# Optimization experiments

Measured on AMD Instinct MI355X. Metric: run time of the kernel, lower is better.

The kernel has to match this reference:

```python
import jax, jax.numpy as jnp
import numpy as np

B, L, D = 8, 4096, 256
G, K = 64, 8          # n_groups, group_size
N = G * K             # 512 slots
H = 8                 # attention heads
EPS = 1e-5

def _ln(x, g, b):
    m = jnp.mean(x, axis=-1, keepdims=True)
    v = jnp.var(x, axis=-1, keepdims=True)
    return (x - m) * jax.lax.rsqrt(v + EPS) * g + b

def _gelu(x):
    return jax.nn.gelu(x, approximate=False)  # torch nn.GELU default = exact erf

def setup_inputs() -> dict:
    key = jax.random.key(0)
    ks = jax.random.split(key, 24)
    s = 0.02
    d = {
        'X': jax.random.normal(ks[0], (B, L, D), jnp.float32),
        'S': jax.random.normal(ks[1], (B, N, D), jnp.float32),
        'Wg':  jax.random.normal(ks[2], (D, G)) * s,
        'Wk':  jax.random.normal(ks[3], (D, K)) * s,
        'Wm1': jax.random.normal(ks[4], (D, 2*D)) * s, 'bm1': jnp.zeros((2*D,)),
        'Wm2': jax.random.normal(ks[5], (2*D, D)) * s, 'bm2': jnp.zeros((D,)),
        'Wgt1': jax.random.normal(ks[6], (D, D)) * s, 'bgt1': jnp.zeros((D,)),
        'Wgt2': jax.random.normal(ks[7], (D, 1)) * s, 'bgt2': jnp.zeros((1,)),
        'Wqkv': jax.random.normal(ks[8], (D, 3*D)) * s, 'bqkv': jnp.zeros((3*D,)),
        'Wo':  jax.random.normal(ks[9], (D, D)) * s, 'bo': jnp.zeros((D,)),
        'aln_g': jnp.ones((D,)), 'aln_b': jnp.zeros((D,)),
        'Wu1': jax.random.normal(ks[10], (2*D, 2*D)) * s, 'bu1': jnp.zeros((2*D,)),
        'Wu2': jax.random.normal(ks[11], (2*D, D)) * s, 'bu2': jnp.zeros((D,)),
        'ln_g': jnp.ones((D,)), 'ln_b': jnp.zeros((D,)),
    }
    return d

def reference(X, S, Wg, Wk, Wm1, bm1, Wm2, bm2, Wgt1, bgt1, Wgt2, bgt2,
              Wqkv, bqkv, Wo, bo, aln_g, aln_b, Wu1, bu1, Wu2, bu2, ln_g, ln_b):
    # --- hierarchical routing (eval path: argmax one-hot) ---
    msg = _gelu(X @ Wm1 + bm1) @ Wm2 + bm2                 # (B,L,D)
    gate = jax.nn.sigmoid(_gelu(X @ Wgt1 + bgt1) @ Wgt2 + bgt2)  # (B,L,1)
    gm = msg * gate
    gidx = jnp.argmax(X @ Wg, axis=-1)                     # (B,L)
    kidx = jnp.argmax(X @ Wk, axis=-1)                     # (B,L)
    idx = gidx * K + kidx                                  # flat slot id in [0,N)
    full = jax.nn.one_hot(idx, N, dtype=X.dtype)           # (B,L,N)
    incoming = jnp.einsum('bln,bld->bnd', full, gm)        # (B,N,D)
    # --- slot self-attention ---
    qkv = S @ Wqkv + bqkv
    q, k, v = jnp.split(qkv, 3, axis=-1)
    dh = D // H
    q = q.reshape(B, N, H, dh); k = k.reshape(B, N, H, dh); v = v.reshape(B, N, H, dh)
    scores = jnp.einsum('bqhd,bkhd->bhqk', q, k) / jnp.sqrt(jnp.asarray(dh, X.dtype))
    attn = jax.nn.softmax(scores, axis=-1)
    o = jnp.einsum('bhqk,bkhd->bqhd', attn, v).reshape(B, N, D) @ Wo + bo
    S1 = _ln(S + o, aln_g, aln_b)
    # --- update ---
    cat = jnp.concatenate([S1, incoming], axis=-1)         # (B,N,2D)
    S2 = S1 + _gelu(cat @ Wu1 + bu1) @ Wu2 + bu2
    return _ln(S2, ln_g, ln_b)
```

## Files before the change

kernel.cpp:

```cpp
#include <hip/hip_runtime.h>

typedef __bf16 bf16_t;
typedef __bf16 bf16x8 __attribute__((ext_vector_type(8)));
typedef __bf16 bf16x4v __attribute__((ext_vector_type(4)));
typedef __bf16 bf16x2v __attribute__((ext_vector_type(2)));
typedef float f32x4 __attribute__((ext_vector_type(4)));
typedef unsigned long long u64;

#define LN_EPS 1e-5f

__device__ __forceinline__ float erf_fast(float a) {
  const float t = fabsf(a);
  const float s = a * a;
  float r;
  if (t > 0.921875f) {
    float u;
    r = fmaf(-1.72853470e-5f, t, 3.83197126e-4f);
    u = fmaf(-3.88396438e-3f, t, 2.42546219e-2f);
    r = fmaf(r, s, u);
    r = fmaf(r, t, 1.06777877e-1f);
    r = fmaf(r, t, -6.37245935e-1f);
    r = fmaf(r, t, -1.28717512e-1f);
    r = fmaf(r, t, t);
    r = 1.0f - __expf(-r);
    r = copysignf(r, a);
  } else {
    r = -5.96761703e-4f;
    r = fmaf(r, s, 4.99119423e-3f);
    r = fmaf(r, s, -2.67681349e-2f);
    r = fmaf(r, s, 1.12819925e-1f);
    r = fmaf(r, s, -3.76125336e-1f);
    r = fmaf(r, s, 1.28379166e-1f);
    r = fmaf(r, a, a);
  }
  return r;
}

__device__ __forceinline__ float gelu_f(float x) {
  const float h = 0.5f * x;
  return fmaf(h, erf_fast(x * 0.70710678118654752f), h);
}

__device__ __forceinline__ void async16(const bf16_t* g, bf16_t* l) {
  __builtin_amdgcn_global_load_lds(
      (const __attribute__((address_space(1))) void*)g,
      (__attribute__((address_space(3))) void*)l, 16, 0, 0);
}

__device__ __forceinline__ int swz(int row, int p) { return p ^ ((row >> 1) & 3); }

__global__ __launch_bounds__(256)
void prep_kernel(const float* __restrict__ X, const float* __restrict__ S,
                 const float* __restrict__ Wg, const float* __restrict__ Wk,
                 const float* __restrict__ Wm1, const float* __restrict__ Wgt1,
                 const float* __restrict__ Wm2, const float* __restrict__ Wqkv,
                 const float* __restrict__ Wo, const float* __restrict__ Wu1,
                 const float* __restrict__ Wu2,
                 bf16_t* __restrict__ Xb, bf16_t* __restrict__ Sb,
                 bf16_t* __restrict__ W1t, bf16_t* __restrict__ W2t,
                 bf16_t* __restrict__ Wqkvt, bf16_t* __restrict__ Wot,
                 bf16_t* __restrict__ Wu1t, bf16_t* __restrict__ Wu2t,
                 float4* __restrict__ zbase)
{
  const int bid = blockIdx.x;
  const int t = threadIdx.x;
  if (bid < 8192) {
    const int i = bid * 256 + t;
    const float4 v = ((const float4*)X)[i];
    bf16x4v o; o[0]=(bf16_t)v.x; o[1]=(bf16_t)v.y; o[2]=(bf16_t)v.z; o[3]=(bf16_t)v.w;
    ((bf16x4v*)Xb)[i] = o;
  } else if (bid < 9216) {
    const int i = (bid - 8192) * 256 + t;
    const float4 v = ((const float4*)S)[i];
    bf16x4v o; o[0]=(bf16_t)v.x; o[1]=(bf16_t)v.y; o[2]=(bf16_t)v.z; o[3]=(bf16_t)v.w;
    ((bf16x4v*)Sb)[i] = o;
  } else if (bid < 10112) {
    const int n = bid - 9216;
    const int k = t;
    float v;
    if (n < 512)      v = Wm1[k * 512 + n];
    else if (n < 768) v = Wgt1[k * 256 + (n - 512)];
    else if (n < 832) v = Wg[k * 64 + (n - 768)];
    else if (n < 840) v = Wk[k * 8 + (n - 832)];
    else              v = 0.f;
    W1t[n * 256 + k] = (bf16_t)v;
  } else if (bid < 10368) {
    const int n = bid - 10112;
    for (int k = t; k < 512; k += 256) W2t[n * 512 + k] = (bf16_t)Wm2[k * 256 + n];
  } else if (bid < 11136) {
    const int n = bid - 10368;
    Wqkvt[n * 256 + t] = (bf16_t)Wqkv[t * 768 + n];
  } else if (bid < 11392) {
    const int n = bid - 11136;
    Wot[n * 256 + t] = (bf16_t)Wo[t * 256 + n];
  } else if (bid < 11904) {
    const int n = bid - 11392;
    for (int k = t; k < 512; k += 256) Wu1t[n * 512 + k] = (bf16_t)Wu1[k * 512 + n];
  } else if (bid < 12160) {
    const int n = bid - 11904;
    for (int k = t; k < 512; k += 256) Wu2t[n * 512 + k] = (bf16_t)Wu2[k * 256 + n];
  } else {
    zbase[(bid - 12160) * 256 + t] = make_float4(0.f, 0.f, 0.f, 0.f);
  }
}

template<int MT, int EPI>
__global__ __launch_bounds__(256)
void gemm_kernel(const bf16_t* __restrict__ A, int lda,
                 const bf16_t* __restrict__ Bt, int K,
                 const float* __restrict__ bias, const float* __restrict__ bias2,
                 void* __restrict__ outp, int ldc,
                 const float* __restrict__ wgt2, float* __restrict__ gatelin,
                 u64* __restrict__ bitmap)
{
  constexpr int BM = MT * 32;
  constexpr int CA = BM * 4;
  const int m0 = blockIdx.x * BM;
  const int by = blockIdx.y;
  const int n0 = by * 128;
  const int t = threadIdx.x;
  const int w = t >> 6;
  const int lane = t & 63;
  const int wr = w >> 1, wc = w & 1;
  const int quad = lane >> 4, l15 = lane & 15;

  __shared__ bf16_t lA[BM * 32];
  __shared__ bf16_t lB[128 * 32];
  __shared__ float sWg[256];
  __shared__ int sKi[BM];

  if constexpr (EPI == 1) {
    if (by >= 4 && by < 6) sWg[t] = wgt2[t];
  }

  f32x4 acc[MT][4];
#pragma unroll
  for (int mt = 0; mt < MT; ++mt)
#pragma unroll
    for (int nt = 0; nt < 4; ++nt)
      acc[mt][nt] = (f32x4){0.f, 0.f, 0.f, 0.f};

  for (int k0 = 0; k0 < K; k0 += 32) {
    if constexpr (CA >= 256) {
#pragma unroll
      for (int i = 0; i < CA / 256; ++i) {
        const int c = i * 256 + t;
        const int row = c >> 2, pp = c & 3;
        async16(A + (size_t)(m0 + row) * lda + k0 + (swz(row, pp) << 3),
                lA + (size_t)(i * 256 + (t & 192)) * 8);
      }
    } else {
      if (t < CA) {
        const int row = t >> 2, pp = t & 3;
        async16(A + (size_t)(m0 + row) * lda + k0 + (swz(row, pp) << 3),
                lA + (size_t)(t & 192) * 8);
      }
    }
#pragma unroll
    for (int i = 0; i < 2; ++i) {
      const int c = i * 256 + t;
      const int row = c >> 2, pp = c & 3;
      async16(Bt + (size_t)(n0 + row) * K + k0 + (swz(row, pp) << 3),
              lB + (size_t)(i * 256 + (t & 192)) * 8);
    }
    __syncthreads();
    bf16x8 af[MT], bfr[4];
#pragma unroll
    for (int mt = 0; mt < MT; ++mt) {
      const int row = wr * MT * 16 + mt * 16 + l15;
      af[mt] = *(const bf16x8*)&lA[row * 32 + (swz(row, quad) << 3)];
    }
#pragma unroll
    for (int nt = 0; nt < 4; ++nt) {
      const int row = wc * 64 + nt * 16 + l15;
      bfr[nt] = *(const bf16x8*)&lB[row * 32 + (swz(row, quad) << 3)];
    }
#pragma unroll
    for (int mt = 0; mt < MT; ++mt)
#pragma unroll
      for (int nt = 0; nt < 4; ++nt)
        acc[mt][nt] = __builtin_amdgcn_mfma_f32_16x16x32_bf16(bfr[nt], af[mt], acc[mt][nt], 0, 0, 0);
    __syncthreads();
  }

  if constexpr (EPI == 1) {
    if (by < 4) {
#pragma unroll
      for (int mt = 0; mt < MT; ++mt) {
        const int row = m0 + wr * MT * 16 + mt * 16 + l15;
#pragma unroll
        for (int nt = 0; nt < 4; ++nt) {
          const int colb = n0 + wc * 64 + nt * 16 + quad * 4;
          const float4 bb = *(const float4*)&bias[colb];
          bf16x4v o;
          o[0] = (bf16_t)(acc[mt][nt][0] + bb.x);
          o[1] = (bf16_t)(acc[mt][nt][1] + bb.y);
          o[2] = (bf16_t)(acc[mt][nt][2] + bb.z);
          o[3] = (bf16_t)(acc[mt][nt][3] + bb.w);
          *(bf16x4v*)&((bf16_t*)outp)[(size_t)row * 512 + colb] = o;
        }
      }
    } else if (by < 6) {
#pragma unroll
      for (int mt = 0; mt < MT; ++mt) {
        const int row = m0 + wr * MT * 16 + mt * 16 + l15;
        float part = 0.f;
#pragma unroll
        for (int nt = 0; nt < 4; ++nt) {
          const int colb = n0 + wc * 64 + nt * 16 + quad * 4;
          const int c = colb - 512;
          const float4 bb = *(const float4*)&bias2[c];
          part = fmaf(gelu_f(acc[mt][nt][0] + bb.x), sWg[c + 0], part);
          part = fmaf(gelu_f(acc[mt][nt][1] + bb.y), sWg[c + 1], part);
          part = fmaf(gelu_f(acc[mt][nt][2] + bb.z), sWg[c + 2], part);
          part = fmaf(gelu_f(acc[mt][nt][3] + bb.w), sWg[c + 3], part);
        }
        part += __shfl_xor(part, 16, 64);
        part += __shfl_xor(part, 32, 64);
        if (lane < 16) atomicAdd(&gatelin[row], part);
      }
    } else {
      int bi[MT];
#pragma unroll
      for (int mt = 0; mt < MT; ++mt) {
        if (wc == 0) {
          float mv = -1e30f; int mi = 0;
#pragma unroll
          for (int nt = 0; nt < 4; ++nt)
#pragma unroll
            for (int j = 0; j < 4; ++j) {
              const int gc = nt * 16 + quad * 4 + j;
              const float v = acc[mt][nt][j];
              if (v > mv || (v == mv && gc < mi)) { mv = v; mi = gc; }
            }
#pragma unroll
          for (int off = 16; off <= 32; off <<= 1) {
            const float ov = __shfl_xor(mv, off, 64);
            const int oi = __shfl_xor(mi, off, 64);
            if (ov > mv || (ov == mv && oi < mi)) { mv = ov; mi = oi; }
          }
          bi[mt] = mi;
        } else {
          float mv = -1e30f; int mi = 0;
          if (quad < 2) {
#pragma unroll
            for (int j = 0; j < 4; ++j) {
              const int kc = quad * 4 + j;
              const float v = acc[mt][0][j];
              if (v > mv || (v == mv && kc < mi)) { mv = v; mi = kc; }
            }
          }
#pragma unroll
          for (int off = 16; off <= 32; off <<= 1) {
            const float ov = __shfl_xor(mv, off, 64);
            const int oi = __shfl_xor(mi, off, 64);
            if (ov > mv || (ov == mv && oi < mi)) { mv = ov; mi = oi; }
          }
          if (lane < 16) sKi[wr * MT * 16 + mt * 16 + l15] = mi;
        }
      }
      __syncthreads();
      if (wc == 0 && lane < 16) {
#pragma unroll
        for (int mt = 0; mt < MT; ++mt) {
          const int rl = wr * MT * 16 + mt * 16 + l15;
          const int row = m0 + rl;
          const int idx = bi[mt] * 8 + sKi[rl];
          const int b = row >> 12, tok = row & 4095;
          atomicOr(&bitmap[(size_t)(b * 512 + idx) * 64 + (tok >> 6)],
                   1ull << (tok & 63));
        }
      }
    }
  } else {
#pragma unroll
    for (int mt = 0; mt < MT; ++mt) {
      const int row = m0 + wr * MT * 16 + mt * 16 + l15;
#pragma unroll
      for (int nt = 0; nt < 4; ++nt) {
        const int colb = n0 + wc * 64 + nt * 16 + quad * 4;
        const float4 bb = *(const float4*)&bias[colb];
        bf16x4v o;
        o[0]=(bf16_t)gelu_f(acc[mt][nt][0]+bb.x); o[1]=(bf16_t)gelu_f(acc[mt][nt][1]+bb.y);
        o[2]=(bf16_t)gelu_f(acc[mt][nt][2]+bb.z); o[3]=(bf16_t)gelu_f(acc[mt][nt][3]+bb.w);
        *(bf16x4v*)&((bf16_t*)outp)[(size_t)row * ldc + colb] = o;
      }
    }
  }
}

__global__ __launch_bounds__(256)
void gemm_pair_kernel(const bf16_t* __restrict__ H, const bf16_t* __restrict__ W2t,
                      const float* __restrict__ bm2, const float* __restrict__ sumg,
                      float* __restrict__ incom,
                      const bf16_t* __restrict__ Sb, const bf16_t* __restrict__ Wqkvt,
                      const float* __restrict__ bqkv, bf16_t* __restrict__ qkvb)
{
  int id = blockIdx.x;
  const bool first = id < 256;
  if (!first) id -= 256;
  const bf16_t* A  = first ? H : Sb;
  const bf16_t* Bt = first ? W2t : Wqkvt;
  const float* bias = first ? bm2 : bqkv;
  const int lda = first ? 512 : 256;
  const int K   = first ? 512 : 256;
  const int ldc = first ? 256 : 768;
  const int m0 = (id & 127) * 32;
  const int n0 = (id >> 7) * 128;
  const int t = threadIdx.x;
  const int w = t >> 6;
  const int lane = t & 63;
  const int wr = w >> 1, wc = w & 1;
  const int quad = lane >> 4, l15 = lane & 15;

  __shared__ bf16_t lA[32 * 32];
  __shared__ bf16_t lB[128 * 32];

  f32x4 acc[4];
#pragma unroll
  for (int nt = 0; nt < 4; ++nt) acc[nt] = (f32x4){0.f, 0.f, 0.f, 0.f};

  for (int k0 = 0; k0 < K; k0 += 32) {
    if (t < 128) {
      const int row = t >> 2, pp = t & 3;
      async16(A + (size_t)(m0 + row) * lda + k0 + (swz(row, pp) << 3),
              lA + (size_t)(t & 192) * 8);
    }
#pragma unroll
    for (int i = 0; i < 2; ++i) {
      const int c = i * 256 + t;
      const int row = c >> 2, pp = c & 3;
      async16(Bt + (size_t)(n0 + row) * K + k0 + (swz(row, pp) << 3),
              lB + (size_t)(i * 256 + (t & 192)) * 8);
    }
    __syncthreads();
    bf16x8 af, bfr[4];
    const int arow = wr * 16 + l15;
    af = *(const bf16x8*)&lA[arow * 32 + (swz(arow, quad) << 3)];
#pragma unroll
    for (int nt = 0; nt < 4; ++nt) {
      const int row = wc * 64 + nt * 16 + l15;
      bfr[nt] = *(const bf16x8*)&lB[row * 32 + (swz(row, quad) << 3)];
    }
#pragma unroll
    for (int nt = 0; nt < 4; ++nt)
      acc[nt] = __builtin_amdgcn_mfma_f32_16x16x32_bf16(bfr[nt], af, acc[nt], 0, 0, 0);
    __syncthreads();
  }

  const int row = m0 + wr * 16 + l15;
  if (first) {
    const float gt = sumg[row];
#pragma unroll
    for (int nt = 0; nt < 4; ++nt) {
      const int colb = n0 + wc * 64 + nt * 16 + quad * 4;
      const float4 bb = *(const float4*)&bias[colb];
      *(float4*)&incom[(size_t)row * ldc + colb] =
          make_float4(fmaf(gt, bb.x, acc[nt][0]), fmaf(gt, bb.y, acc[nt][1]),
                      fmaf(gt, bb.z, acc[nt][2]), fmaf(gt, bb.w, acc[nt][3]));
    }
  } else {
#pragma unroll
    for (int nt = 0; nt < 4; ++nt) {
      const int colb = n0 + wc * 64 + nt * 16 + quad * 4;
      const float4 bb = *(const float4*)&bias[colb];
      bf16x4v o; o[0]=(bf16_t)(acc[nt][0]+bb.x); o[1]=(bf16_t)(acc[nt][1]+bb.y);
      o[2]=(bf16_t)(acc[nt][2]+bb.z); o[3]=(bf16_t)(acc[nt][3]+bb.w);
      *(bf16x4v*)&qkvb[(size_t)row * ldc + colb] = o;
    }
  }
}

__global__ __launch_bounds__(256)
void gather_kernel(const bf16_t* __restrict__ h1, const float* __restrict__ gatelin,
                   const float* __restrict__ bgt2, const u64* __restrict__ bitmap,
                   bf16_t* __restrict__ H, float* __restrict__ sumg)
{
  const int bs = blockIdx.x;
  const int b = bs >> 9;
  const int t = threadIdx.x;
  __shared__ u64 sw[64];
  if (t < 64) sw[t] = bitmap[(size_t)bs * 64 + t];
  __syncthreads();
  const float bg = bgt2[0];
  float a0 = 0.f, a1 = 0.f, sg = 0.f;
  for (int wd = 0; wd < 64; ++wd) {
    u64 word = sw[wd];
    while (word) {
      const int bit = __builtin_ctzll(word);
      word &= word - 1;
      const int l = (b << 12) + (wd << 6) + bit;
      const float g = 1.0f / (1.0f + __expf(-(gatelin[l] + bg)));
      const bf16x2v hv = *(const bf16x2v*)&h1[(size_t)l * 512 + t * 2];
      a0 = fmaf(g, gelu_f((float)hv[0]), a0);
      a1 = fmaf(g, gelu_f((float)hv[1]), a1);
      sg += g;
    }
  }
  bf16x2v o; o[0] = (bf16_t)a0; o[1] = (bf16_t)a1;
  *(bf16x2v*)&H[(size_t)bs * 512 + t * 2] = o;
  if (t == 0) sumg[bs] = sg;
}

__global__ __launch_bounds__(256)
void attn_kernel(const bf16_t* __restrict__ qkv, bf16_t* __restrict__ obuf)
{
  const int bid = blockIdx.x;
  const int qc = bid & 15;
  const int h = (bid >> 4) & 7;
  const int b = bid >> 7;
  const int t = threadIdx.x;
  const int w = t >> 6, lane = t & 63;
  const int quad = lane >> 4, l15 = lane & 15;

  __shared__ bf16_t sP[32 * 520];
  __shared__ bf16_t sVt[32 * 264];
  __shared__ float sL[32];

  bf16x8 qf[2];
#pragma unroll
  for (int mt = 0; mt < 2; ++mt) {
    const int row = b * 512 + qc * 32 + mt * 16 + l15;
    qf[mt] = *(const bf16x8*)&qkv[(size_t)row * 768 + h * 32 + quad * 8];
  }
  const float scale = 0.17677669529663687f;
  for (int kt = w; kt < 32; kt += 4) {
    const int key = b * 512 + kt * 16 + l15;
    const bf16x8 kf = *(const bf16x8*)&qkv[(size_t)key * 768 + 256 + h * 32 + quad * 8];
#pragma unroll
    for (int mt = 0; mt < 2; ++mt) {
      f32x4 c = (f32x4){0.f, 0.f, 0.f, 0.f};
      c = __builtin_amdgcn_mfma_f32_16x16x32_bf16(qf[mt], kf, c, 0, 0, 0);
#pragma unroll
      for (int r = 0; r < 4; ++r)
        sP[(mt * 16 + quad * 4 + r) * 520 + kt * 16 + l15] = (bf16_t)(c[r] * scale);
    }
  }
  __syncthreads();

#pragma unroll
  for (int ri = 0; ri < 8; ++ri) {
    const int row = w * 8 + ri;
    const bf16x8 sv = *(const bf16x8*)&sP[row * 520 + lane * 8];
    float sval[8];
    float mx = -1e30f;
#pragma unroll
    for (int j = 0; j < 8; ++j) { sval[j] = (float)sv[j]; mx = fmaxf(mx, sval[j]); }
#pragma unroll
    for (int off = 32; off; off >>= 1) mx = fmaxf(mx, __shfl_xor(mx, off, 64));
    float sum = 0.f;
    bf16x8 pv;
#pragma unroll
    for (int j = 0; j < 8; ++j) { const float e = __expf(sval[j] - mx); sum += e; pv[j] = (bf16_t)e; }
#pragma unroll
    for (int off = 32; off; off >>= 1) sum += __shfl_xor(sum, off, 64);
    *(bf16x8*)&sP[row * 520 + lane * 8] = pv;
    if (lane == 0) sL[row] = sum;
  }
  __syncthreads();

  const int omt = w >> 1, ont = w & 1;
  f32x4 oacc = (f32x4){0.f, 0.f, 0.f, 0.f};
  for (int half = 0; half < 2; ++half) {
    if (half) __syncthreads();
#pragma unroll
    for (int i = 0; i < 32; ++i) {
      const int el = i * 256 + t;
      const int dh = el & 31, key = el >> 5;
      sVt[dh * 264 + key] = qkv[(size_t)(b * 512 + half * 256 + key) * 768 + 512 + h * 32 + dh];
    }
    __syncthreads();
#pragma unroll
    for (int kt = 0; kt < 8; ++kt) {
      const bf16x8 af = *(const bf16x8*)&sP[(omt * 16 + l15) * 520 + half * 256 + kt * 32 + quad * 8];
      const bf16x8 vf = *(const bf16x8*)&sVt[(ont * 16 + l15) * 264 + kt * 32 + quad * 8];
      oacc = __builtin_amdgcn_mfma_f32_16x16x32_bf16(af, vf, oacc, 0, 0, 0);
    }
  }
#pragma unroll
  for (int r = 0; r < 4; ++r) {
    const int row = omt * 16 + quad * 4 + r;
    const float val = oacc[r] / sL[row];
    obuf[(size_t)(b * 512 + qc * 32 + row) * 256 + h * 32 + ont * 16 + l15] = (bf16_t)val;
  }
}

__global__ __launch_bounds__(256)
void wo_ln1_kernel(const bf16_t* __restrict__ obuf, const bf16_t* __restrict__ Wot,
                   const float* __restrict__ bo, const float* __restrict__ S,
                   const float* __restrict__ incom, const float* __restrict__ g,
                   const float* __restrict__ bb, float* __restrict__ S1f,
                   bf16_t* __restrict__ A4)
{
  const int m0 = blockIdx.x * 16;
  const int t = threadIdx.x;
  const int w = t >> 6, lane = t & 63;
  const int quad = lane >> 4, l15 = lane & 15;

  __shared__ bf16_t lA[16 * 32];
  __shared__ bf16_t lB[256 * 32];
  __shared__ float sSum[4][16];
  __shared__ float sSq[4][16];

  f32x4 acc[4];
#pragma unroll
  for (int nt = 0; nt < 4; ++nt) acc[nt] = (f32x4){0.f, 0.f, 0.f, 0.f};

  for (int k0 = 0; k0 < 256; k0 += 32) {
    if (t < 64) {
      const int row = t >> 2, pp = t & 3;
      async16(obuf + (size_t)(m0 + row) * 256 + k0 + (swz(row, pp) << 3), lA);
    }
#pragma unroll
    for (int i = 0; i < 4; ++i) {
      const int c = i * 256 + t;
      const int row = c >> 2, pp = c & 3;
      async16(Wot + (size_t)row * 256 + k0 + (swz(row, pp) << 3),
              lB + (size_t)(i * 256 + (t & 192)) * 8);
    }
    __syncthreads();
    const bf16x8 af = *(const bf16x8*)&lA[l15 * 32 + (swz(l15, quad) << 3)];
#pragma unroll
    for (int nt = 0; nt < 4; ++nt) {
      const int row = w * 64 + nt * 16 + l15;
      const bf16x8 bfr = *(const bf16x8*)&lB[row * 32 + (swz(row, quad) << 3)];
      acc[nt] = __builtin_amdgcn_mfma_f32_16x16x32_bf16(bfr, af, acc[nt], 0, 0, 0);
    }
    __syncthreads();
  }

  const int row = m0 + l15;
  float sum = 0.f, sq = 0.f;
#pragma unroll
  for (int nt = 0; nt < 4; ++nt) {
    const int colb = w * 64 + nt * 16 + quad * 4;
    const float4 bv = *(const float4*)&bo[colb];
    const float4 sv = *(const float4*)&S[(size_t)row * 256 + colb];
    float x0 = acc[nt][0] + bv.x + sv.x, x1 = acc[nt][1] + bv.y + sv.y;
    float x2 = acc[nt][2] + bv.z + sv.z, x3 = acc[nt][3] + bv.w + sv.w;
    acc[nt][0] = x0; acc[nt][1] = x1; acc[nt][2] = x2; acc[nt][3] = x3;
    sum += x0 + x1 + x2 + x3;
    sq += x0*x0 + x1*x1 + x2*x2 + x3*x3;
  }
  sum += __shfl_xor(sum, 16, 64); sum += __shfl_xor(sum, 32, 64);
  sq  += __shfl_xor(sq, 16, 64);  sq  += __shfl_xor(sq, 32, 64);
  if (lane < 16) { sSum[w][l15] = sum; sSq[w][l15] = sq; }
  __syncthreads();
  const float tot = sSum[0][l15] + sSum[1][l15] + sSum[2][l15] + sSum[3][l15];
  const float tq  = sSq[0][l15] + sSq[1][l15] + sSq[2][l15] + sSq[3][l15];
  const float mean = tot * 0.00390625f;
  const float var = tq * 0.00390625f - mean * mean;
  const float rstd = rsqrtf(var + LN_EPS);
#pragma unroll
  for (int nt = 0; nt < 4; ++nt) {
    const int colb = w * 64 + nt * 16 + quad * 4;
    const float4 gg = *(const float4*)&g[colb];
    const float4 bv = *(const float4*)&bb[colb];
    const float y0 = (acc[nt][0]-mean)*rstd*gg.x + bv.x;
    const float y1 = (acc[nt][1]-mean)*rstd*gg.y + bv.y;
    const float y2 = (acc[nt][2]-mean)*rstd*gg.z + bv.z;
    const float y3 = (acc[nt][3]-mean)*rstd*gg.w + bv.w;
    *(float4*)&S1f[(size_t)row * 256 + colb] = make_float4(y0, y1, y2, y3);
    bf16x4v yb; yb[0]=(bf16_t)y0; yb[1]=(bf16_t)y1; yb[2]=(bf16_t)y2; yb[3]=(bf16_t)y3;
    *(bf16x4v*)&A4[(size_t)row * 512 + colb] = yb;
    const float4 ic = *(const float4*)&incom[(size_t)row * 256 + colb];
    bf16x4v ib; ib[0]=(bf16_t)ic.x; ib[1]=(bf16_t)ic.y; ib[2]=(bf16_t)ic.z; ib[3]=(bf16_t)ic.w;
    *(bf16x4v*)&A4[(size_t)row * 512 + 256 + colb] = ib;
  }
}

__global__ __launch_bounds__(256)
void wu2_ln2_kernel(const bf16_t* __restrict__ U, const bf16_t* __restrict__ Wu2t,
                    const float* __restrict__ bu2, const float* __restrict__ S1f,
                    const float* __restrict__ g, const float* __restrict__ bb,
                    float* __restrict__ out)
{
  const int m0 = blockIdx.x * 16;
  const int t = threadIdx.x;
  const int w = t >> 6, lane = t & 63;
  const int quad = lane >> 4, l15 = lane & 15;

  __shared__ bf16_t lA[16 * 32];
  __shared__ bf16_t lB[256 * 32];
  __shared__ float sSum[4][16];
  __shared__ float sSq[4][16];

  f32x4 acc[4];
#pragma unroll
  for (int nt = 0; nt < 4; ++nt) acc[nt] = (f32x4){0.f, 0.f, 0.f, 0.f};

  for (int k0 = 0; k0 < 512; k0 += 32) {
    if (t < 64) {
      const int row = t >> 2, pp = t & 3;
      async16(U + (size_t)(m0 + row) * 512 + k0 + (swz(row, pp) << 3), lA);
    }
#pragma unroll
    for (int i = 0; i < 4; ++i) {
      const int c = i * 256 + t;
      const int row = c >> 2, pp = c & 3;
      async16(Wu2t + (size_t)row * 512 + k0 + (swz(row, pp) << 3),
              lB + (size_t)(i * 256 + (t & 192)) * 8);
    }
    __syncthreads();
    const bf16x8 af = *(const bf16x8*)&lA[l15 * 32 + (swz(l15, quad) << 3)];
#pragma unroll
    for (int nt = 0; nt < 4; ++nt) {
      const int row = w * 64 + nt * 16 + l15;
      const bf16x8 bfr = *(const bf16x8*)&lB[row * 32 + (swz(row, quad) << 3)];
      acc[nt] = __builtin_amdgcn_mfma_f32_16x16x32_bf16(bfr, af, acc[nt], 0, 0, 0);
    }
    __syncthreads();
  }

  const int row = m0 + l15;
  float sum = 0.f, sq = 0.f;
#pragma unroll
  for (int nt = 0; nt < 4; ++nt) {
    const int colb = w * 64 + nt * 16 + quad * 4;
    const float4 bv = *(const float4*)&bu2[colb];
    const float4 sv = *(const float4*)&S1f[(size_t)row * 256 + colb];
    float x0 = acc[nt][0] + bv.x + sv.x, x1 = acc[nt][1] + bv.y + sv.y;
    float x2 = acc[nt][2] + bv.z + sv.z, x3 = acc[nt][3] + bv.w + sv.w;
    acc[nt][0] = x0; acc[nt][1] = x1; acc[nt][2] = x2; acc[nt][3] = x3;
    sum += x0 + x1 + x2 + x3;
    sq += x0*x0 + x1*x1 + x2*x2 + x3*x3;
  }
  sum += __shfl_xor(sum, 16, 64); sum += __shfl_xor(sum, 32, 64);
  sq  += __shfl_xor(sq, 16, 64);  sq  += __shfl_xor(sq, 32, 64);
  if (lane < 16) { sSum[w][l15] = sum; sSq[w][l15] = sq; }
  __syncthreads();
  const float tot = sSum[0][l15] + sSum[1][l15] + sSum[2][l15] + sSum[3][l15];
  const float tq  = sSq[0][l15] + sSq[1][l15] + sSq[2][l15] + sSq[3][l15];
  const float mean = tot * 0.00390625f;
  const float var = tq * 0.00390625f - mean * mean;
  const float rstd = rsqrtf(var + LN_EPS);
#pragma unroll
  for (int nt = 0; nt < 4; ++nt) {
    const int colb = w * 64 + nt * 16 + quad * 4;
    const float4 gg = *(const float4*)&g[colb];
    const float4 bv = *(const float4*)&bb[colb];
    *(float4*)&out[(size_t)row * 256 + colb] = make_float4(
        (acc[nt][0]-mean)*rstd*gg.x + bv.x, (acc[nt][1]-mean)*rstd*gg.y + bv.y,
        (acc[nt][2]-mean)*rstd*gg.z + bv.z, (acc[nt][3]-mean)*rstd*gg.w + bv.w);
  }
}

extern "C" void kernel_launch(void* const* d_in, const int* in_sizes, int n_in,
                              void* d_out, int out_size, void* d_ws, size_t ws_size,
                              hipStream_t stream)
{
  (void)in_sizes; (void)n_in; (void)out_size; (void)ws_size;
  const float* X    = (const float*)d_in[0];
  const float* S    = (const float*)d_in[1];
  const float* Wg   = (const float*)d_in[2];
  const float* Wk   = (const float*)d_in[3];
  const float* Wm1  = (const float*)d_in[4];
  const float* bm1  = (const float*)d_in[5];
  const float* Wm2  = (const float*)d_in[6];
  const float* bm2  = (const float*)d_in[7];
  const float* Wgt1 = (const float*)d_in[8];
  const float* bgt1 = (const float*)d_in[9];
  const float* Wgt2 = (const float*)d_in[10];
  const float* bgt2 = (const float*)d_in[11];
  const float* Wqkv = (const float*)d_in[12];
  const float* bqkv = (const float*)d_in[13];
  const float* Wo   = (const float*)d_in[14];
  const float* bo   = (const float*)d_in[15];
  const float* alng = (const float*)d_in[16];
  const float* alnb = (const float*)d_in[17];
  const float* Wu1  = (const float*)d_in[18];
  const float* bu1  = (const float*)d_in[19];
  const float* Wu2  = (const float*)d_in[20];
  const float* bu2  = (const float*)d_in[21];
  const float* lng  = (const float*)d_in[22];
  const float* lnb  = (const float*)d_in[23];

  char* p = (char*)d_ws;
  auto carve = [&](size_t bytes) { char* r = p; p += bytes; return r; };
  bf16_t* Xb    = (bf16_t*)carve(16777216);
  bf16_t* Sb    = (bf16_t*)carve(2097152);
  bf16_t* W1t   = (bf16_t*)carve(458752);
  bf16_t* W2t   = (bf16_t*)carve(262144);
  bf16_t* Wqkvt = (bf16_t*)carve(393216);
  bf16_t* Wot   = (bf16_t*)carve(131072);
  bf16_t* Wu1t  = (bf16_t*)carve(524288);
  bf16_t* Wu2t  = (bf16_t*)carve(262144);
  bf16_t* h1    = (bf16_t*)carve(33554432);
  u64*    bitmap  = (u64*)carve(2097152);
  float*  gatelin = (float*)carve(131072);
  float*  incom = (float*)carve(4194304);
  bf16_t* qkvb  = (bf16_t*)carve(6291456);
  bf16_t* obuf  = (bf16_t*)carve(2097152);
  float*  S1f   = (float*)carve(4194304);
  bf16_t* A4    = (bf16_t*)carve(4194304);
  bf16_t* U     = (bf16_t*)carve(4194304);
  float*  sumg  = (float*)carve(16384);
  bf16_t* H = U;

  prep_kernel<<<12704, 256, 0, stream>>>(X, S, Wg, Wk, Wm1, Wgt1, Wm2, Wqkv, Wo, Wu1, Wu2,
                                         Xb, Sb, W1t, W2t, Wqkvt, Wot, Wu1t, Wu2t,
                                         (float4*)bitmap);
  gemm_kernel<2,1><<<dim3(512,7), 256, 0, stream>>>(Xb, 256, W1t, 256, bm1, bgt1, h1, 512,
                                                    Wgt2, gatelin, bitmap);
  gather_kernel<<<4096, 256, 0, stream>>>(h1, gatelin, bgt2, bitmap, H, sumg);
  gemm_pair_kernel<<<1024, 256, 0, stream>>>(H, W2t, bm2, sumg, incom,
                                             Sb, Wqkvt, bqkv, qkvb);
  attn_kernel<<<1024, 256, 0, stream>>>(qkvb, obuf);
  wo_ln1_kernel<<<256, 256, 0, stream>>>(obuf, Wot, bo, S, incom, alng, alnb, S1f, A4);
  gemm_kernel<1,5><<<dim3(128,4), 256, 0, stream>>>(A4, 512, Wu1t, 512, bu1, nullptr, U, 512,
                                                    nullptr, nullptr, nullptr);
  wu2_ln2_kernel<<<256, 256, 0, stream>>>(U, Wu2t, bu2, S1f, lng, lnb, (float*)d_out);
}
```

Before: 264.7 us.

## Fuse Wo+LN1, Wu1 GEMM and Wu2+LN2 into one slot tail kernel; tile weight transposes

Merges the Wo projection with LN1, the Wu1 GEMM with GELU, and the Wu2 projection with LN2 into a single kernel per 16-row slot block. Intermediates (S1, concat, U) stay in shared memory and registers instead of going through global memory, which also removes two kernel launches. Separately, weight transposes in the prep kernel now go through 64x64 shared-memory tiles so both reads and writes are coalesced, replacing one-block-per-column strided reads. The trade-off is that the fused tail runs only 256 blocks, each doing all three GEMMs serially, which limits parallelism on the Wu1 stage.

```diff
diff --git a/kernel.cpp b/kernel.cpp
--- a/kernel.cpp
+++ b/kernel.cpp
@@ -64,6 +64,23 @@
 {
   const int bid = blockIdx.x;
   const int t = threadIdx.x;
+  __shared__ float sT[64][65];
+
+  auto do_tr = [&](const float* src, int C, bf16_t* dst, int ld, int tiles_c, int j) {
+    const int r0 = (j / tiles_c) * 64, c0 = (j % tiles_c) * 64;
+#pragma unroll 4
+    for (int i = 0; i < 16; ++i) {
+      const int rr = i * 4 + (t >> 6), cc = t & 63;
+      sT[rr][cc] = src[(size_t)(r0 + rr) * C + c0 + cc];
+    }
+    __syncthreads();
+#pragma unroll 4
+    for (int i = 0; i < 16; ++i) {
+      const int rr = i * 4 + (t >> 6), cc = t & 63;
+      dst[(size_t)(c0 + rr) * ld + r0 + cc] = (bf16_t)sT[cc][rr];
+    }
+  };
+
   if (bid < 8192) {
     const int i = bid * 256 + t;
     const float4 v = ((const float4*)X)[i];
@@ -74,33 +91,30 @@
     const float4 v = ((const float4*)S)[i];
     bf16x4v o; o[0]=(bf16_t)v.x; o[1]=(bf16_t)v.y; o[2]=(bf16_t)v.z; o[3]=(bf16_t)v.w;
     ((bf16x4v*)Sb)[i] = o;
-  } else if (bid < 10112) {
-    const int n = bid - 9216;
-    const int k = t;
-    float v;
-    if (n < 512)      v = Wm1[k * 512 + n];
-    else if (n < 768) v = Wgt1[k * 256 + (n - 512)];
-    else if (n < 832) v = Wg[k * 64 + (n - 768)];
-    else if (n < 840) v = Wk[k * 8 + (n - 832)];
-    else              v = 0.f;
-    W1t[n * 256 + k] = (bf16_t)v;
-  } else if (bid < 10368) {
-    const int n = bid - 10112;
-    for (int k = t; k < 512; k += 256) W2t[n * 512 + k] = (bf16_t)Wm2[k * 256 + n];
-  } else if (bid < 11136) {
-    const int n = bid - 10368;
-    Wqkvt[n * 256 + t] = (bf16_t)Wqkv[t * 768 + n];
-  } else if (bid < 11392) {
-    const int n = bid - 11136;
-    Wot[n * 256 + t] = (bf16_t)Wo[t * 256 + n];
-  } else if (bid < 11904) {
-    const int n = bid - 11392;
-    for (int k = t; k < 512; k += 256) Wu1t[n * 512 + k] = (bf16_t)Wu1[k * 512 + n];
-  } else if (bid < 12160) {
-    const int n = bid - 11904;
-    for (int k = t; k < 512; k += 256) Wu2t[n * 512 + k] = (bf16_t)Wu2[k * 256 + n];
+  } else if (bid < 9248) {
+    do_tr(Wm1, 512, W1t, 256, 8, bid - 9216);
+  } else if (bid < 9264) {
+    do_tr(Wgt1, 256, W1t + 512 * 256, 256, 4, bid - 9248);
+  } else if (bid < 9268) {
+    do_tr(Wg, 64, W1t + 768 * 256, 256, 1, bid - 9264);
+  } else if (bid < 9269) {
+#pragma unroll
+    for (int i = 0; i < 8; ++i)
+      W1t[(832 + i) * 256 + t] = (bf16_t)Wk[t * 8 + i];
+    for (int r = 0; r < 56; ++r)
+      W1t[(840 + r) * 256 + t] = (bf16_t)0.f;
+  } else if (bid < 9301) {
+    do_tr(Wm2, 256, W2t, 512, 4, bid - 9269);
+  } else if (bid < 9349) {
+    do_tr(Wqkv, 768, Wqkvt, 256, 12, bid - 9301);
+  } else if (bid < 9365) {
+    do_tr(Wo, 256, Wot, 256, 4, bid - 9349);
+  } else if (bid < 9429) {
+    do_tr(Wu1, 512, Wu1t, 512, 8, bid - 9365);
+  } else if (bid < 9461) {
+    do_tr(Wu2, 256, Wu2t, 512, 4, bid - 9429);
   } else {
-    zbase[(bid - 12160) * 256 + t] = make_float4(0.f, 0.f, 0.f, 0.f);
+    zbase[(bid - 9461) * 256 + t] = make_float4(0.f, 0.f, 0.f, 0.f);
   }
 }
 
@@ -270,20 +284,6 @@
           atomicOr(&bitmap[(size_t)(b * 512 + idx) * 64 + (tok >> 6)],
                    1ull << (tok & 63));
         }
-      }
-    }
-  } else {
-#pragma unroll
-    for (int mt = 0; mt < MT; ++mt) {
-      const int row = m0 + wr * MT * 16 + mt * 16 + l15;
-#pragma unroll
-      for (int nt = 0; nt < 4; ++nt) {
-        const int colb = n0 + wc * 64 + nt * 16 + quad * 4;
-        const float4 bb = *(const float4*)&bias[colb];
-        bf16x4v o;
-        o[0]=(bf16_t)gelu_f(acc[mt][nt][0]+bb.x); o[1]=(bf16_t)gelu_f(acc[mt][nt][1]+bb.y);
-        o[2]=(bf16_t)gelu_f(acc[mt][nt][2]+bb.z); o[3]=(bf16_t)gelu_f(acc[mt][nt][3]+bb.w);
-        *(bf16x4v*)&((bf16_t*)outp)[(size_t)row * ldc + colb] = o;
       }
     }
   }
@@ -486,26 +486,28 @@
 }
 
 __global__ __launch_bounds__(256)
-void wo_ln1_kernel(const bf16_t* __restrict__ obuf, const bf16_t* __restrict__ Wot,
-                   const float* __restrict__ bo, const float* __restrict__ S,
-                   const float* __restrict__ incom, const float* __restrict__ g,
-                   const float* __restrict__ bb, float* __restrict__ S1f,
-                   bf16_t* __restrict__ A4)
+void slot_tail_kernel(const bf16_t* __restrict__ obuf, const bf16_t* __restrict__ Wot,
+                      const float* __restrict__ bo, const float* __restrict__ S,
+                      const float* __restrict__ incom,
+                      const float* __restrict__ ag, const float* __restrict__ ab,
+                      const bf16_t* __restrict__ Wu1t, const float* __restrict__ bu1,
+                      const bf16_t* __restrict__ Wu2t, const float* __restrict__ bu2,
+                      const float* __restrict__ lg, const float* __restrict__ lb,
+                      float* __restrict__ out)
 {
   const int m0 = blockIdx.x * 16;
   const int t = threadIdx.x;
   const int w = t >> 6, lane = t & 63;
   const int quad = lane >> 4, l15 = lane & 15;
 
+  __shared__ bf16_t lB[512 * 32];
   __shared__ bf16_t lA[16 * 32];
-  __shared__ bf16_t lB[256 * 32];
-  __shared__ float sSum[4][16];
-  __shared__ float sSq[4][16];
+  __shared__ bf16_t sA[16 * 520];
+  __shared__ float sSum[4][16], sSq[4][16];
 
   f32x4 acc[4];
 #pragma unroll
   for (int nt = 0; nt < 4; ++nt) acc[nt] = (f32x4){0.f, 0.f, 0.f, 0.f};
-
   for (int k0 = 0; k0 < 256; k0 += 32) {
     if (t < 64) {
       const int row = t >> 2, pp = t & 3;
@@ -546,102 +548,122 @@
   sq  += __shfl_xor(sq, 16, 64);  sq  += __shfl_xor(sq, 32, 64);
   if (lane < 16) { sSum[w][l15] = sum; sSq[w][l15] = sq; }
   __syncthreads();
-  const float tot = sSum[0][l15] + sSum[1][l15] + sSum[2][l15] + sSum[3][l15];
-  const float tq  = sSq[0][l15] + sSq[1][l15] + sSq[2][l15] + sSq[3][l15];
-  const float mean = tot * 0.00390625f;
-  const float var = tq * 0.00390625f - mean * mean;
-  const float rstd = rsqrtf(var + LN_EPS);
-#pragma unroll
-  for (int nt = 0; nt < 4; ++nt) {
-    const int colb = w * 64 + nt * 16 + quad * 4;
-    const float4 gg = *(const float4*)&g[colb];
-    const float4 bv = *(const float4*)&bb[colb];
-    const float y0 = (acc[nt][0]-mean)*rstd*gg.x + bv.x;
-    const float y1 = (acc[nt][1]-mean)*rstd*gg.y + bv.y;
-    const float y2 = (acc[nt][2]-mean)*rstd*gg.z + bv.z;
-    const float y3 = (acc[nt][3]-mean)*rstd*gg.w + bv.w;
-    *(float4*)&S1f[(size_t)row * 256 + colb] = make_float4(y0, y1, y2, y3);
-    bf16x4v yb; yb[0]=(bf16_t)y0; yb[1]=(bf16_t)y1; yb[2]=(bf16_t)y2; yb[3]=(bf16_t)y3;
-    *(bf16x4v*)&A4[(size_t)row * 512 + colb] = yb;
-    const float4 ic = *(const float4*)&incom[(size_t)row * 256 + colb];
-    bf16x4v ib; ib[0]=(bf16_t)ic.x; ib[1]=(bf16_t)ic.y; ib[2]=(bf16_t)ic.z; ib[3]=(bf16_t)ic.w;
-    *(bf16x4v*)&A4[(size_t)row * 512 + 256 + colb] = ib;
-  }
-}
-
-__global__ __launch_bounds__(256)
-void wu2_ln2_kernel(const bf16_t* __restrict__ U, const bf16_t* __restrict__ Wu2t,
-                    const float* __restrict__ bu2, const float* __restrict__ S1f,
-                    const float* __restrict__ g, const float* __restrict__ bb,
-                    float* __restrict__ out)
-{
-  const int m0 = blockIdx.x * 16;
-  const int t = threadIdx.x;
-  const int w = t >> 6, lane = t & 63;
-  const int quad = lane >> 4, l15 = lane & 15;
-
-  __shared__ bf16_t lA[16 * 32];
-  __shared__ bf16_t lB[256 * 32];
-  __shared__ float sSum[4][16];
-  __shared__ float sSq[4][16];
-
-  f32x4 acc[4];
-#pragma unroll
-  for (int nt = 0; nt < 4; ++nt) acc[nt] = (f32x4){0.f, 0.f, 0.f, 0.f};
-
+  {
+    const float tot = sSum[0][l15] + sSum[1][l15] + sSum[2][l15] + sSum[3][l15];
+    const float tq  = sSq[0][l15] + sSq[1][l15] + sSq[2][l15] + sSq[3][l15];
+    const float mean = tot * 0.00390625f;
+    const float var = tq * 0.00390625f - mean * mean;
+    const float rstd = rsqrtf(var + LN_EPS);
+#pragma unroll
+    for (int nt = 0; nt < 4; ++nt) {
+      const int colb = w * 64 + nt * 16 + quad * 4;
+      const float4 gg = *(const float4*)&ag[colb];
+      const float4 bv = *(const float4*)&ab[colb];
+      acc[nt][0] = (acc[nt][0]-mean)*rstd*gg.x + bv.x;
+      acc[nt][1] = (acc[nt][1]-mean)*rstd*gg.y + bv.y;
+      acc[nt][2] = (acc[nt][2]-mean)*rstd*gg.z + bv.z;
+      acc[nt][3] = (acc[nt][3]-mean)*rstd*gg.w + bv.w;
+      bf16x4v yb; yb[0]=(bf16_t)acc[nt][0]; yb[1]=(bf16_t)acc[nt][1];
+      yb[2]=(bf16_t)acc[nt][2]; yb[3]=(bf16_t)acc[nt][3];
+      *(bf16x4v*)&sA[l15 * 520 + colb] = yb;
+    }
+  }
+#pragma unroll
+  for (int i = 0; i < 16; ++i) {
+    const int idx = i * 256 + t;
+    const int rr = idx >> 8, cc = idx & 255;
+    sA[rr * 520 + 256 + cc] = (bf16_t)incom[(size_t)(m0 + rr) * 256 + cc];
+  }
+  float y[16];
+#pragma unroll
+  for (int nt = 0; nt < 4; ++nt)
+#pragma unroll
+    for (int j = 0; j < 4; ++j) y[nt * 4 + j] = acc[nt][j];
+  __syncthreads();
+
+  f32x4 acc2[8];
+#pragma unroll
+  for (int nt = 0; nt < 8; ++nt) acc2[nt] = (f32x4){0.f, 0.f, 0.f, 0.f};
   for (int k0 = 0; k0 < 512; k0 += 32) {
-    if (t < 64) {
-      const int row = t >> 2, pp = t & 3;
-      async16(U + (size_t)(m0 + row) * 512 + k0 + (swz(row, pp) << 3), lA);
-    }
+#pragma unroll
+    for (int i = 0; i < 8; ++i) {
+      const int c = i * 256 + t;
+      const int rown = c >> 2, pp = c & 3;
+      async16(Wu1t + (size_t)rown * 512 + k0 + (swz(rown, pp) << 3),
+              lB + (size_t)(i * 256 + (t & 192)) * 8);
+    }
+    __syncthreads();
+    const bf16x8 af = *(const bf16x8*)&sA[l15 * 520 + k0 + quad * 8];
+#pragma unroll
+    for (int nt = 0; nt < 8; ++nt) {
+      const int rown = w * 128 + nt * 16 + l15;
+      const bf16x8 bfr = *(const bf16x8*)&lB[rown * 32 + (swz(rown, quad) << 3)];
+      acc2[nt] = __builtin_amdgcn_mfma_f32_16x16x32_bf16(bfr, af, acc2[nt], 0, 0, 0);
+    }
+    __syncthreads();
+  }
+#pragma unroll
+  for (int nt = 0; nt < 8; ++nt) {
+    const int colb = w * 128 + nt * 16 + quad * 4;
+    const float4 bv = *(const float4*)&bu1[colb];
+    bf16x4v o;
+    o[0] = (bf16_t)gelu_f(acc2[nt][0] + bv.x);
+    o[1] = (bf16_t)gelu_f(acc2[nt][1] + bv.y);
+    o[2] = (bf16_t)gelu_f(acc2[nt][2] + bv.z);
+    o[3] = (bf16_t)gelu_f(acc2[nt][3] + bv.w);
+    *(bf16x4v*)&sA[l15 * 520 + colb] = o;
+  }
+  __syncthreads();
+
+  f32x4 acc3[4];
+#pragma unroll
+  for (int nt = 0; nt < 4; ++nt) acc3[nt] = (f32x4){0.f, 0.f, 0.f, 0.f};
+  for (int k0 = 0; k0 < 512; k0 += 32) {
 #pragma unroll
     for (int i = 0; i < 4; ++i) {
       const int c = i * 256 + t;
-      const int row = c >> 2, pp = c & 3;
-      async16(Wu2t + (size_t)row * 512 + k0 + (swz(row, pp) << 3),
+      const int rown = c >> 2, pp = c & 3;
+      async16(Wu2t + (size_t)rown * 512 + k0 + (swz(rown, pp) << 3),
               lB + (size_t)(i * 256 + (t & 192)) * 8);
     }
     __syncthreads();
-    const bf16x8 af = *(const bf16x8*)&lA[l15 * 32 + (swz(l15, quad) << 3)];
+    const bf16x8 af = *(const bf16x8*)&sA[l15 * 520 + k0 + quad * 8];
 #pragma unroll
     for (int nt = 0; nt < 4; ++nt) {
-      const int row = w * 64 + nt * 16 + l15;
-      const bf16x8 bfr = *(const bf16x8*)&lB[row * 32 + (swz(row, quad) << 3)];
-      acc[nt] = __builtin_amdgcn_mfma_f32_16x16x32_bf16(bfr, af, acc[nt], 0, 0, 0);
-    }
-    __syncthreads();
-  }
-
-  const int row = m0 + l15;
-  float sum = 0.f, sq = 0.f;
+      const int rown = w * 64 + nt * 16 + l15;
+      const bf16x8 bfr = *(const bf16x8*)&lB[rown * 32 + (swz(rown, quad) << 3)];
+      acc3[nt] = __builtin_amdgcn_mfma_f32_16x16x32_bf16(bfr, af, acc3[nt], 0, 0, 0);
+    }
+    __syncthreads();
+  }
+  float sum2 = 0.f, sq2 = 0.f;
 #pragma unroll
   for (int nt = 0; nt < 4; ++nt) {
     const int colb = w * 64 + nt * 16 + quad * 4;
     const float4 bv = *(const float4*)&bu2[colb];
-    const float4 sv = *(const float4*)&S1f[(size_t)row * 256 + colb];
-    float x0 = acc[nt][0] + bv.x + sv.x, x1 = acc[nt][1] + bv.y + sv.y;
-    float x2 = acc[nt][2] + bv.z + sv.z, x3 = acc[nt][3] + bv.w + sv.w;
-    acc[nt][0] = x0; acc[nt][1] = x1; acc[nt][2] = x2; acc[nt][3] = x3;
-    sum += x0 + x1 + x2 + x3;
-    sq += x0*x0 + x1*x1 + x2*x2 + x3*x3;
-  }
-  sum += __shfl_xor(sum, 16, 64); sum += __shfl_xor(sum, 32, 64);
-  sq  += __shfl_xor(sq, 16, 64);  sq  += __shfl_xor(sq, 32, 64);
-  if (lane < 16) { sSum[w][l15] = sum; sSq[w][l15] = sq; }
+    float x0 = acc3[nt][0] + bv.x + y[nt*4+0], x1 = acc3[nt][1] + bv.y + y[nt*4+1];
+    float x2 = acc3[nt][2] + bv.z + y[nt*4+2], x3 = acc3[nt][3] + bv.w + y[nt*4+3];
+    acc3[nt][0] = x0; acc3[nt][1] = x1; acc3[nt][2] = x2; acc3[nt][3] = x3;
+    sum2 += x0 + x1 + x2 + x3;
+    sq2 += x0*x0 + x1*x1 + x2*x2 + x3*x3;
+  }
+  sum2 += __shfl_xor(sum2, 16, 64); sum2 += __shfl_xor(sum2, 32, 64);
+  sq2  += __shfl_xor(sq2, 16, 64);  sq2  += __shfl_xor(sq2, 32, 64);
+  if (lane < 16) { sSum[w][l15] = sum2; sSq[w][l15] = sq2; }
   __syncthreads();
-  const float tot = sSum[0][l15] + sSum[1][l15] + sSum[2][l15] + sSum[3][l15];
-  const float tq  = sSq[0][l15] + sSq[1][l15] + sSq[2][l15] + sSq[3][l15];
-  const float mean = tot * 0.00390625f;
-  const float var = tq * 0.00390625f - mean * mean;
-  const float rstd = rsqrtf(var + LN_EPS);
+  const float tot2 = sSum[0][l15] + sSum[1][l15] + sSum[2][l15] + sSum[3][l15];
+  const float tq2  = sSq[0][l15] + sSq[1][l15] + sSq[2][l15] + sSq[3][l15];
+  const float mean2 = tot2 * 0.00390625f;
+  const float var2 = tq2 * 0.00390625f - mean2 * mean2;
+  const float rstd2 = rsqrtf(var2 + LN_EPS);
 #pragma unroll
   for (int nt = 0; nt < 4; ++nt) {
     const int colb = w * 64 + nt * 16 + quad * 4;
-    const float4 gg = *(const float4*)&g[colb];
-    const float4 bv = *(const float4*)&bb[colb];
+    const float4 gg = *(const float4*)&lg[colb];
+    const float4 bv = *(const float4*)&lb[colb];
     *(float4*)&out[(size_t)row * 256 + colb] = make_float4(
-        (acc[nt][0]-mean)*rstd*gg.x + bv.x, (acc[nt][1]-mean)*rstd*gg.y + bv.y,
-        (acc[nt][2]-mean)*rstd*gg.z + bv.z, (acc[nt][3]-mean)*rstd*gg.w + bv.w);
+        (acc3[nt][0]-mean2)*rstd2*gg.x + bv.x, (acc3[nt][1]-mean2)*rstd2*gg.y + bv.y,
+        (acc3[nt][2]-mean2)*rstd2*gg.z + bv.z, (acc3[nt][3]-mean2)*rstd2*gg.w + bv.w);
   }
 }
 
@@ -691,13 +713,10 @@
   float*  incom = (float*)carve(4194304);
   bf16_t* qkvb  = (bf16_t*)carve(6291456);
   bf16_t* obuf  = (bf16_t*)carve(2097152);
-  float*  S1f   = (float*)carve(4194304);
-  bf16_t* A4    = (bf16_t*)carve(4194304);
-  bf16_t* U     = (bf16_t*)carve(4194304);
+  bf16_t* H     = (bf16_t*)carve(4194304);
   float*  sumg  = (float*)carve(16384);
-  bf16_t* H = U;
-
-  prep_kernel<<<12704, 256, 0, stream>>>(X, S, Wg, Wk, Wm1, Wgt1, Wm2, Wqkv, Wo, Wu1, Wu2,
+
+  prep_kernel<<<10005, 256, 0, stream>>>(X, S, Wg, Wk, Wm1, Wgt1, Wm2, Wqkv, Wo, Wu1, Wu2,
                                          Xb, Sb, W1t, W2t, Wqkvt, Wot, Wu1t, Wu2t,
                                          (float4*)bitmap);
   gemm_kernel<2,1><<<dim3(512,7), 256, 0, stream>>>(Xb, 256, W1t, 256, bm1, bgt1, h1, 512,
@@ -706,8 +725,7 @@
   gemm_pair_kernel<<<1024, 256, 0, stream>>>(H, W2t, bm2, sumg, incom,
                                              Sb, Wqkvt, bqkv, qkvb);
   attn_kernel<<<1024, 256, 0, stream>>>(qkvb, obuf);
-  wo_ln1_kernel<<<256, 256, 0, stream>>>(obuf, Wot, bo, S, incom, alng, alnb, S1f, A4);
-  gemm_kernel<1,5><<<dim3(128,4), 256, 0, stream>>>(A4, 512, Wu1t, 512, bu1, nullptr, U, 512,
-                                                    nullptr, nullptr, nullptr);
-  wu2_ln2_kernel<<<256, 256, 0, stream>>>(U, Wu2t, bu2, S1f, lng, lnb, (float*)d_out);
-}
+  slot_tail_kernel<<<256, 256, 0, stream>>>(obuf, Wot, bo, S, incom, alng, alnb,
+                                            Wu1t, bu1, Wu2t, bu2, lng, lnb,
+                                            (float*)d_out);
+}
```

New measurement: 263.4 us. Within noise of the previous version (-0.5%).
